# Kernel optimization log

Hardware: AMD Instinct MI355X
Metric: run time of the kernel (lower is better)

Reference implementation:

```python
import jax, jax.numpy as jnp
import numpy as np

N_NODES = 50000
N_EDGES = 1600000
NFEAT = 512
NHID = 64
H1 = 8      # nheads[0]
H2 = 1      # nheads[1]
NCLASS = 16
ALPHA = 0.2  # leaky_relu negative slope


def setup_inputs() -> dict:
    key = jax.random.key(0)
    ks = jax.random.split(key, 6)
    x = jax.random.normal(ks[0], (N_NODES, NFEAT), jnp.float32)
    edge_index = jax.random.randint(ks[1], (2, N_EDGES), 0, N_NODES, jnp.int32)

    def glorot(k, shape):
        fan_in, fan_out = shape[-2], shape[-1]
        std = (2.0 / (fan_in + fan_out)) ** 0.5
        return jax.random.normal(k, shape, jnp.float32) * std

    W1 = glorot(ks[2], (H1, NFEAT, NHID))
    a1 = jax.random.normal(ks[3], (H1, 2 * NHID), jnp.float32) * 0.1
    W2 = glorot(ks[4], (H2, NHID * H1, NCLASS))
    a2 = jax.random.normal(ks[5], (H2, 2 * NCLASS), jnp.float32) * 0.1
    return {"x": x, "edge_index": edge_index, "W1": W1, "a1": a1, "W2": W2, "a2": a2}


def _spgat_head(x, W, a, src, dst, n_nodes, apply_elu):
    # Sparse GAT head (pyGAT SpGraphAttentionLayer, eval mode / no dropout).
    h = x @ W                              # [N, F']
    f = W.shape[1]
    # a . [h_src || h_dst] decomposed into per-node scores (same math, no [E,2F'] concat)
    s_src = h @ a[:f]                      # [N]
    s_dst = h @ a[f:]                      # [N]
    logits = s_src[src] + s_dst[dst]       # [E]
    e = jnp.exp(-jax.nn.leaky_relu(logits, ALPHA))  # edge_e = exp(-leakyrelu(...)) > 0
    rowsum = jax.ops.segment_sum(e, src, num_segments=n_nodes)            # [N]
    agg = jax.ops.segment_sum(e[:, None] * h[dst], src, num_segments=n_nodes)  # [N, F']
    h_prime = agg / rowsum[:, None]
    return jax.nn.elu(h_prime) if apply_elu else h_prime


def reference(x, edge_index, W1, a1, W2, a2):
    src, dst = edge_index[0], edge_index[1]
    n = x.shape[0]
    # Layer 1: H1 heads, concat=True (elu inside each head), concatenated on features
    h = jnp.concatenate(
        [_spgat_head(x, W1[i], a1[i], src, dst, n, True) for i in range(W1.shape[0])],
        axis=1,
    )  # [N, H1*NHID]
    # Layer 2: H2 heads, concat=False, stacked then averaged
    outs = jnp.stack(
        [_spgat_head(h, W2[i], a2[i], src, dst, n, False) for i in range(W2.shape[0])],
        axis=2,
    )  # [N, NCLASS, H2]
    out = jnp.mean(outs, axis=2)
    return jax.nn.log_softmax(jax.nn.elu(out), axis=1)
```

## Files before the change

### kernel.cpp

```cpp
#include <hip/hip_runtime.h>

#define NN 50000
#define NE 1600000
#define NFEAT 512
#define NHID 64
#define H1 8
#define NCLASS 16
#define ALPHA 0.2f

#define BUCKETS 391
#define CAP 6144
#define EPB 4096
#define PASSA_BLKS 391
#define PASSB_BLKS 391
#define PACK_BLKS 1024
#define PACK2_BLKS 32
#define X8_BLKS 6250
#define GEMMB 391
#define NROW_PAD 50048

typedef __attribute__((ext_vector_type(8))) short short8;
typedef __attribute__((ext_vector_type(4))) float floatx4;
typedef __attribute__((ext_vector_type(2))) float floatx2;
typedef __attribute__((ext_vector_type(2))) long longx2;

__device__ __forceinline__ float elu_f(float x) { return x > 0.0f ? x : expf(x) - 1.0f; }
__device__ __forceinline__ float edge_w(float logit) {
    return expf(-fmaxf(logit, ALPHA * logit));
}
__device__ __forceinline__ ushort f2bf(float f) {
    uint u = __float_as_uint(f);
    return (ushort)((u + 0x7FFFu + ((u >> 16) & 1)) >> 16);
}
__device__ __forceinline__ uint packbf2(float lo, float hi) {
    return (uint)f2bf(lo) | ((uint)f2bf(hi) << 16);
}
__device__ __forceinline__ float bf2f(ushort v) { return __uint_as_float((uint)v << 16); }
__device__ __forceinline__ unsigned char f2fp8(float v) {
    return (unsigned char)(__builtin_amdgcn_cvt_pk_fp8_f32(v, v, 0, false) & 0xFF);
}
__device__ __forceinline__ uint pack4fp8(float a, float b, float c, float d) {
    uint u = __builtin_amdgcn_cvt_pk_fp8_f32(a, b, 0, false);
    return __builtin_amdgcn_cvt_pk_fp8_f32(c, d, u, true);
}

#define GLD16(g, l)                                                              \
    __builtin_amdgcn_global_load_lds(                                            \
        (const __attribute__((address_space(1))) unsigned int*)(g),              \
        (__attribute__((address_space(3))) unsigned int*)(l), 16, 0, 0)

__device__ __forceinline__ int scan256x(int v, int tid, int* wsum, int* tot) {
    int s = v;
#pragma unroll
    for (int o = 1; o < 64; o <<= 1) {
        int u = __shfl_up(s, o);
        if ((tid & 63) >= o) s += u;
    }
    __syncthreads();
    if ((tid & 63) == 63) wsum[tid >> 6] = s;
    __syncthreads();
    int off = 0, t = 0;
#pragma unroll
    for (int i = 0; i < 4; i++) {
        int x = wsum[i];
        if (i < (tid >> 6)) off += x;
        t += x;
    }
    *tot = t;
    return s - v + off;
}

__device__ __forceinline__ int scan512x(int v, int tid, int* wsum, int* tot) {
    int s = v;
#pragma unroll
    for (int o = 1; o < 64; o <<= 1) {
        int u = __shfl_up(s, o);
        if ((tid & 63) >= o) s += u;
    }
    __syncthreads();
    if ((tid & 63) == 63) wsum[tid >> 6] = s;
    __syncthreads();
    int off = 0, t = 0;
#pragma unroll
    for (int i = 0; i < 8; i++) {
        int x = wsum[i];
        if (i < (tid >> 6)) off += x;
        t += x;
    }
    *tot = t;
    return s - v + off;
}

__global__ __launch_bounds__(256) void prep_k(const float* __restrict__ W1,
                                              unsigned char* __restrict__ Wt8,
                                              const float* __restrict__ W2,
                                              ushort* __restrict__ W2tb,
                                              const float* __restrict__ x,
                                              unsigned char* x8,
                                              const int* __restrict__ ei,
                                              int* __restrict__ bucket_cnt,
                                              uint* __restrict__ staging) {
    int b = blockIdx.x;
    if (b < PACK_BLKS) {
        int i = b * 256 + threadIdx.x;
        int c = i >> 9, o = i & 511;
        int c6 = o >> 6, qhi = (o >> 4) & 3, kb = (o >> 3) & 1, bb = o & 7;
        int quad = qhi ^ ((c >> 1) & 3);
        int k = c6 * 64 + kb * 32 + quad * 8 + bb;
        Wt8[i] = f2fp8(W1[((c >> 6) * 512 + k) * 64 + (c & 63)]);
        return;
    }
    if (b < PACK_BLKS + PACK2_BLKS) {
        int i = (b - PACK_BLKS) * 256 + threadIdx.x;
        int c = i >> 9, f = i & 511;
        W2tb[i] = f2bf(W2[f * 16 + c]);
        return;
    }
    if (b < PACK_BLKS + PACK2_BLKS + X8_BLKS) {
        int i = (b - PACK_BLKS - PACK2_BLKS) * 256 + threadIdx.x;
        int row = i >> 5;
        int o0 = (i & 31) * 16;
        int c6 = o0 >> 6;
        int qhi = (o0 >> 4) & 3;
        int quad = qhi ^ ((row >> 1) & 3);
        const float* xp = x + (size_t)row * 512 + c6 * 64 + quad * 8;
        float4 v0 = *(const float4*)xp;
        float4 v1 = *(const float4*)(xp + 4);
        float4 v2 = *(const float4*)(xp + 32);
        float4 v3 = *(const float4*)(xp + 36);
        uint4 ov;
        ov.x = pack4fp8(v0.x, v0.y, v0.z, v0.w);
        ov.y = pack4fp8(v1.x, v1.y, v1.z, v1.w);
        ov.z = pack4fp8(v2.x, v2.y, v2.z, v2.w);
        ov.w = pack4fp8(v3.x, v3.y, v3.z, v3.w);
        *(uint4*)(x8 + (size_t)row * 512 + o0) = ov;
        return;
    }
    __shared__ int histA[BUCKETS];
    __shared__ int exclA[BUCKETS];
    __shared__ int baseA[BUCKETS];
    __shared__ int wsumA[4];
    __shared__ uint ebuf[EPB];
    const int blk = b - PACK_BLKS - PACK2_BLKS - X8_BLKS;
    const int t = threadIdx.x;
    const int e0 = blk * EPB;
    const int cntb = min(EPB, NE - e0);
    for (int i = t; i < BUCKETS; i += 256) histA[i] = 0;
    __syncthreads();
    int br[16]; uint pay[16];
#pragma unroll
    for (int i = 0; i < 16; i++) {
        int e = e0 + i * 256 + t;
        br[i] = -1;
        if (e < NE) {
            int s = ei[e], d = ei[NE + e];
            int bu = s >> 7;
            pay[i] = ((uint)bu << 23) | ((uint)(s & 127) << 16) | (uint)d;
            br[i] = (bu << 12) | atomicAdd(&histA[bu], 1);
        }
    }
    __syncthreads();
    int tot0, tot1;
    int v0 = histA[t];
    int v1 = (t + 256 < BUCKETS) ? histA[t + 256] : 0;
    int p0 = scan256x(v0, t, wsumA, &tot0);
    int p1 = scan256x(v1, t, wsumA, &tot1);
    exclA[t] = p0;
    if (t + 256 < BUCKETS) exclA[t + 256] = p1 + tot0;
    __syncthreads();
    for (int i = t; i < BUCKETS; i += 256) {
        int c = histA[i];
        if (c > 0) baseA[i] = atomicAdd(&bucket_cnt[i], c);
    }
#pragma unroll
    for (int i = 0; i < 16; i++)
        if (br[i] >= 0) ebuf[exclA[br[i] >> 12] + (br[i] & 4095)] = pay[i];
    __syncthreads();
    for (int j = t; j < cntb; j += 256) {
        uint v = ebuf[j];
        int bu = v >> 23;
        int pos = baseA[bu] + (j - exclA[bu]);
        staging[(size_t)bu * CAP + pos] = v;
    }
}

__global__ __launch_bounds__(64) void scan_k(const int* __restrict__ bucket_cnt,
                                             int* __restrict__ bucket_start,
                                             int* __restrict__ rowptr) {
    const int lane = threadIdx.x;
    int c[7]; int s0 = 0;
#pragma unroll
    for (int i = 0; i < 7; i++) {
        int b = lane * 7 + i;
        c[i] = (b < BUCKETS) ? bucket_cnt[b] : 0;
        s0 += c[i];
    }
    int sc = s0;
#pragma unroll
    for (int o = 1; o < 64; o <<= 1) {
        int u = __shfl_up(sc, o);
        if (lane >= o) sc += u;
    }
    int run = sc - s0;
#pragma unroll
    for (int i = 0; i < 7; i++) {
        int b = lane * 7 + i;
        if (b < BUCKETS) bucket_start[b] = run;
        run += c[i];
    }
    if (lane == 63) { bucket_start[BUCKETS] = run; rowptr[NN] = run; }
}

__global__ __launch_bounds__(512) void passb_gemm1_k(const int* __restrict__ bucket_cnt,
                                                     const int* __restrict__ bucket_start,
                                                     const uint* __restrict__ staging,
                                                     ushort* __restrict__ csru,
                                                     int* __restrict__ rowptr,
                                                     const unsigned char* __restrict__ Wt8,
                                                     const float* __restrict__ a1,
                                                     unsigned char* h8x8,
                                                     float* __restrict__ s1s,
                                                     float* __restrict__ s1d) {
    __shared__ unsigned char shmem[40960];
    const int tid = threadIdx.x;

    if (blockIdx.x < PASSB_BLKS) {
        int* hist2 = (int*)shmem;
        int* excl2 = hist2 + 128;
        int* cur2 = excl2 + 128;
        int* wsum2 = cur2 + 128;
        const int b = blockIdx.x;
        const int cnt = bucket_cnt[b];
        const int sbase = bucket_start[b];
        const uint* sg = staging + (size_t)b * CAP;
        if (tid < 128) { hist2[tid] = 0; cur2[tid] = 0; }
        __syncthreads();
        for (int e = tid; e < cnt; e += 512) atomicAdd(&hist2[(sg[e] >> 16) & 127], 1);
        __syncthreads();
        int v = (tid < 128) ? hist2[tid] : 0;
        int tot;
        int ex = scan512x(v, tid, wsum2, &tot);
        if (tid < 128) {
            excl2[tid] = ex;
            int n = b * 128 + tid;
            if (n < NN) rowptr[n] = sbase + ex;
        }
        __syncthreads();
        for (int e = tid; e < cnt; e += 512) {
            uint u = sg[e];
            int sl = (u >> 16) & 127;
            int pos = excl2[sl] + atomicAdd(&cur2[sl], 1);
            csru[sbase + pos] = (ushort)(u & 0xFFFF);
        }
        return;
    }

    unsigned char* As = shmem;
    unsigned char* Bs = shmem + 8192;
    const int gb = blockIdx.x - PASSB_BLKS;
    const int row0 = gb * 128;
    const int wv = tid >> 6, lane = tid & 63;
    const int l16 = lane & 15, quad = lane >> 4;
    const int qoff = ((quad ^ ((l16 >> 1) & 3)) << 4);
    const int mA = wv * 16 + (lane >> 2);
    const int offA = (lane & 3) * 16;
    const unsigned char* gA = h8x8 + (size_t)(row0 + mA) * 512 + offA;
    const unsigned char* gB0 = Wt8 + (size_t)(0 * 128 + mA) * 512 + offA;
    const unsigned char* gB1 = Wt8 + (size_t)(1 * 128 + mA) * 512 + offA;
    const unsigned char* gB2 = Wt8 + (size_t)(2 * 128 + mA) * 512 + offA;
    const unsigned char* gB3 = Wt8 + (size_t)(3 * 128 + mA) * 512 + offA;

    floatx4 acc[32];
#pragma unroll
    for (int ct = 0; ct < 32; ct++) acc[ct] = (floatx4){0.f, 0.f, 0.f, 0.f};

    for (int k0 = 0; k0 < 512; k0 += 64) {
        GLD16(gA + k0, As + wv * 1024);
        GLD16(gB0 + k0, Bs + wv * 1024);
        GLD16(gB1 + k0, Bs + 8192 + wv * 1024);
        GLD16(gB2 + k0, Bs + 16384 + wv * 1024);
        GLD16(gB3 + k0, Bs + 24576 + wv * 1024);
        __syncthreads();
        longx2 av = *(const longx2*)(As + (wv * 16 + l16) * 64 + qoff);
        const unsigned char* bp = Bs + l16 * 64 + qoff;
#pragma unroll
        for (int ct = 0; ct < 32; ct++) {
            longx2 bv = *(const longx2*)(bp + ct * 1024);
            acc[ct] = __builtin_amdgcn_mfma_f32_16x16x32_fp8_fp8(av.x, bv.x, acc[ct], 0, 0, 0);
            acc[ct] = __builtin_amdgcn_mfma_f32_16x16x32_fp8_fp8(av.y, bv.y, acc[ct], 0, 0, 0);
        }
        __syncthreads();
    }

    const int rbase = row0 + wv * 16 + quad * 4;
#pragma unroll
    for (int hh = 0; hh < 8; hh++) {
        float ss[4] = {0.f, 0.f, 0.f, 0.f}, sd[4] = {0.f, 0.f, 0.f, 0.f};
#pragma unroll
        for (int c4 = 0; c4 < 4; c4++) {
            int ct = hh * 4 + c4;
            int colg = ct * 16 + l16;
            float avs = a1[hh * 128 + c4 * 16 + l16];
            float avd = a1[hh * 128 + 64 + c4 * 16 + l16];
#pragma unroll
            for (int r = 0; r < 4; r++) {
                float v = acc[ct][r];
                ss[r] += v * avs;
                sd[r] += v * avd;
                int row = rbase + r;
                if (row < NN) h8x8[(size_t)row * 512 + colg] = f2fp8(v);
            }
        }
#pragma unroll
        for (int r = 0; r < 4; r++) {
            float a_ = ss[r], b_ = sd[r];
#pragma unroll
            for (int o = 1; o < 16; o <<= 1) {
                a_ += __shfl_xor(a_, o);
                b_ += __shfl_xor(b_, o);
            }
            int row = rbase + r;
            if (l16 == 0 && row < NN) {
                s1s[row * 8 + hh] = a_;
                s1d[row * 8 + hh] = b_;
            }
        }
    }
}

__global__ __launch_bounds__(256) void agg1f_k(const int* __restrict__ rowptr,
                                               const ushort* __restrict__ csru,
                                               const float* __restrict__ s1s,
                                               const float* __restrict__ s1d,
                                               const uint2* __restrict__ hb8,
                                               const ushort* __restrict__ W2tb,
                                               const float* __restrict__ a2,
                                               ushort* __restrict__ h2b,
                                               float* __restrict__ s2s,
                                               float* __restrict__ s2d) {
    __shared__ ushort Ash[16 * 512];
    const int tid = threadIdx.x;
    const int wv = tid >> 6, lane = tid & 63;
    const int n0 = blockIdx.x * 4;
    const int n = n0 + wv;
    const int head8 = lane >> 3;
    const int esub = lane & 7;
    const int beg = rowptr[n];
    const int deg = rowptr[n + 1] - beg;
    const float ssrc = s1s[n * 8 + head8];
    floatx2 acc[4] = {};
    float rsum = 0.f;

    int k = 0;
    for (; k + 8 <= deg; k += 8) {
        int dA = csru[beg + k + esub];
        float wA = edge_w(ssrc + s1d[dA * 8 + head8]);
        rsum += wA;
        int dj[8];
#pragma unroll
        for (int j = 0; j < 8; j++) dj[j] = __shfl(dA, j);
        uint2 v[8];
#pragma unroll
        for (int j = 0; j < 8; j++) v[j] = hb8[(uint)dj[j] * 64 + lane];
#pragma unroll
        for (int j = 0; j < 8; j++) {
            float wj = __shfl(wA, (head8 << 3) + j);
            floatx2 w2 = (floatx2){wj, wj};
            acc[0] += w2 * __builtin_amdgcn_cvt_pk_f32_fp8(v[j].x, false);
            acc[1] += w2 * __builtin_amdgcn_cvt_pk_f32_fp8(v[j].x, true);
            acc[2] += w2 * __builtin_amdgcn_cvt_pk_f32_fp8(v[j].y, false);
            acc[3] += w2 * __builtin_amdgcn_cvt_pk_f32_fp8(v[j].y, true);
        }
    }
    if (k < deg) {
        int jc = min(k + esub, deg - 1);
        int dwj = csru[beg + jc];
        float w = edge_w(ssrc + s1d[dwj * 8 + head8]);
        if (k + esub >= deg) w = 0.f;
        rsum += w;
        int rem = deg - k;
        for (int j = 0; j < rem; j++) {
            int djs = __shfl(dwj, j);
            uint2 vv = hb8[(uint)djs * 64 + lane];
            float wj = __shfl(w, (head8 << 3) + j);
            floatx2 w2 = (floatx2){wj, wj};
            acc[0] += w2 * __builtin_amdgcn_cvt_pk_f32_fp8(vv.x, false);
            acc[1] += w2 * __builtin_amdgcn_cvt_pk_f32_fp8(vv.x, true);
            acc[2] += w2 * __builtin_amdgcn_cvt_pk_f32_fp8(vv.y, false);
            acc[3] += w2 * __builtin_amdgcn_cvt_pk_f32_fp8(vv.y, true);
        }
    }

    rsum += __shfl_xor(rsum, 1);
    rsum += __shfl_xor(rsum, 2);
    rsum += __shfl_xor(rsum, 4);
    float inv = 1.0f / rsum;
    uint4 o;
    o.x = packbf2(elu_f(acc[0][0] * inv), elu_f(acc[0][1] * inv));
    o.y = packbf2(elu_f(acc[1][0] * inv), elu_f(acc[1][1] * inv));
    o.z = packbf2(elu_f(acc[2][0] * inv), elu_f(acc[2][1] * inv));
    o.w = packbf2(elu_f(acc[3][0] * inv), elu_f(acc[3][1] * inv));
    *(uint4*)(Ash + wv * 512 + lane * 8) = o;
    __syncthreads();

    if (wv == 0) {
        const int l16 = lane & 15, q = lane >> 4;
        floatx4 c2 = (floatx4){0.f, 0.f, 0.f, 0.f};
#pragma unroll
        for (int s = 0; s < 16; s++) {
            short8 af = *(const short8*)(Ash + l16 * 512 + s * 32 + q * 8);
            short8 bf = *(const short8*)(W2tb + l16 * 512 + s * 32 + q * 8);
            c2 = __builtin_amdgcn_mfma_f32_16x16x32_bf16(af, bf, c2, 0, 0, 0);
        }
        if (q == 0) {
#pragma unroll
            for (int r = 0; r < 4; r++) h2b[(size_t)(n0 + r) * 16 + l16] = f2bf(c2[r]);
        }
#pragma unroll
        for (int r = 0; r < 4; r++) {
            float ssv = c2[r] * a2[l16];
            float sdv = c2[r] * a2[16 + l16];
#pragma unroll
            for (int oo = 1; oo < 16; oo <<= 1) {
                ssv += __shfl_xor(ssv, oo);
                sdv += __shfl_xor(sdv, oo);
            }
            if (lane == 0) { s2s[n0 + r] = ssv; s2d[n0 + r] = sdv; }
        }
    }
}

__global__ __launch_bounds__(256) void agg2_k(const int* __restrict__ rowptr,
                                              const ushort* __restrict__ csru,
                                              const float* __restrict__ s2s,
                                              const float* __restrict__ s2d,
                                              const ushort* __restrict__ h2b,
                                              float* __restrict__ out) {
    const int n = (blockIdx.x * 256 + threadIdx.x) >> 6;
    const int lane = threadIdx.x & 63;
    if (n >= NN) return;
    const int beg = rowptr[n], end = rowptr[n + 1];
    const float sn = s2s[n];
    const int sub = lane >> 4, f = lane & 15;
    float acc = 0.f, rsum = 0.f;
    int e = beg + sub;
    for (; e + 12 < end; e += 16) {
        int d0 = csru[e], d1 = csru[e + 4], d2 = csru[e + 8], d3 = csru[e + 12];
        float t0 = s2d[d0], t1 = s2d[d1], t2 = s2d[d2], t3 = s2d[d3];
        float g0 = bf2f(h2b[(uint)d0 * 16 + f]), g1 = bf2f(h2b[(uint)d1 * 16 + f]);
        float g2 = bf2f(h2b[(uint)d2 * 16 + f]), g3 = bf2f(h2b[(uint)d3 * 16 + f]);
        float w0 = edge_w(sn + t0), w1 = edge_w(sn + t1);
        float w2 = edge_w(sn + t2), w3 = edge_w(sn + t3);
        acc += w0 * g0 + w1 * g1 + w2 * g2 + w3 * g3;
        rsum += w0 + w1 + w2 + w3;
    }
    for (; e < end; e += 4) {
        int d0 = csru[e];
        float w0 = edge_w(sn + s2d[d0]);
        acc += w0 * bf2f(h2b[(uint)d0 * 16 + f]);
        rsum += w0;
    }
    acc += __shfl_down(acc, 32);
    acc += __shfl_down(acc, 16);
    rsum += __shfl_down(rsum, 32);
    rsum += __shfl_down(rsum, 16);
    if (lane < 16) {
        float v = elu_f(acc / rsum);
        float m = v;
#pragma unroll
        for (int o = 8; o > 0; o >>= 1) m = fmaxf(m, __shfl_xor(m, o));
        float ex = expf(v - m), s = ex;
#pragma unroll
        for (int o = 8; o > 0; o >>= 1) s += __shfl_xor(s, o);
        out[(size_t)n * 16 + f] = v - (logf(s) + m);
    }
}

extern "C" void kernel_launch(void* const* d_in, const int* in_sizes, int n_in,
                              void* d_out, int out_size, void* d_ws, size_t ws_size,
                              hipStream_t stream) {
    const float* x  = (const float*)d_in[0];
    const int*   ei = (const int*)d_in[1];
    const float* W1 = (const float*)d_in[2];
    const float* a1 = (const float*)d_in[3];
    const float* W2 = (const float*)d_in[4];
    const float* a2 = (const float*)d_in[5];
    float* out = (float*)d_out;

    unsigned char* h8  = (unsigned char*)d_ws;
    unsigned char* Wt8 = h8 + (size_t)NROW_PAD * 512;
    ushort* W2tb  = (ushort*)(Wt8 + 512 * 512);
    float* s1s    = (float*)(W2tb + 8192);
    float* s1d    = s1s + (size_t)NN * H1;
    int* rowptr   = (int*)(s1d + (size_t)NN * H1);
    int* bucket_cnt   = rowptr + 50056;
    int* bucket_start = bucket_cnt + 512;
    ushort* csru  = (ushort*)(bucket_start + 512);
    ushort* h2b   = csru + NE;
    float* s2s    = (float*)(h2b + (size_t)NN * 16);
    float* s2d    = s2s + NN;
    uint* staging = (uint*)(s2d + NN);

    hipMemsetAsync(bucket_cnt, 0, 512 * sizeof(int), stream);

    prep_k<<<PACK_BLKS + PACK2_BLKS + X8_BLKS + PASSA_BLKS, 256, 0, stream>>>(
        W1, Wt8, W2, W2tb, x, h8, ei, bucket_cnt, staging);
    scan_k<<<1, 64, 0, stream>>>(bucket_cnt, bucket_start, rowptr);
    passb_gemm1_k<<<PASSB_BLKS + GEMMB, 512, 0, stream>>>(bucket_cnt, bucket_start,
                                                          staging, csru, rowptr,
                                                          Wt8, a1, h8, s1s, s1d);
    agg1f_k<<<NN / 4, 256, 0, stream>>>(rowptr, csru, s1s, s1d,
                                        (const uint2*)h8, W2tb, a2, h2b, s2s, s2d);
    agg2_k<<<(NN + 3) / 4, 256, 0, stream>>>(rowptr, csru, s2s, s2d, h2b, out);
}
```

Measured before the change: 401.4 us.

## Double-buffer edge gathers in layer-1 aggregation, swizzle LDS, use fast exp/log

The layer-1 aggregation loop is software-pipelined. It prefetches the next group of 8 neighbour indices, attention scores and fp8 feature rows into a second register buffer while the current group is accumulated, so gather latency overlaps with the FMA work. The LDS tile that feeds the second-layer MFMA now uses an XOR-swizzled layout to reduce bank conflicts on the strided row reads. expf and logf are also replaced by the __expf and __logf intrinsics. In exchange, the kernel uses more registers for the doubled gather buffers, which may lower occupancy, and the fast math intrinsics are slightly less accurate.

```diff
diff --git a/kernel.cpp b/kernel.cpp
--- a/kernel.cpp
+++ b/kernel.cpp
@@ -24,9 +24,9 @@
 typedef __attribute__((ext_vector_type(2))) float floatx2;
 typedef __attribute__((ext_vector_type(2))) long longx2;
 
-__device__ __forceinline__ float elu_f(float x) { return x > 0.0f ? x : expf(x) - 1.0f; }
+__device__ __forceinline__ float elu_f(float x) { return x > 0.0f ? x : __expf(x) - 1.0f; }
 __device__ __forceinline__ float edge_w(float logit) {
-    return expf(-fmaxf(logit, ALPHA * logit));
+    return __expf(-fmaxf(logit, ALPHA * logit));
 }
 __device__ __forceinline__ ushort f2bf(float f) {
     uint u = __float_as_uint(f);
@@ -328,6 +328,30 @@
     }
 }
 
+#define PREF8(gg, dN, twN, vN)                                        \
+    {                                                                 \
+        int idx_ = ((gg) < G) ? beg + (gg) * 8 + esub : beg;          \
+        dN = csru[idx_];                                              \
+        twN = s1d[dN * 8 + head8];                                    \
+        _Pragma("unroll") for (int j_ = 0; j_ < 8; j_++) {            \
+            int dj_ = __shfl(dN, j_);                                 \
+            vN[j_] = hb8[(uint)dj_ * 64 + lane];                      \
+        }                                                             \
+    }
+
+#define COMP8(wC, vC)                                                             \
+    {                                                                             \
+        rsum += wC;                                                               \
+        _Pragma("unroll") for (int j_ = 0; j_ < 8; j_++) {                        \
+            float wj_ = __shfl(wC, hb + j_);                                      \
+            floatx2 w2_ = (floatx2){wj_, wj_};                                    \
+            acc[0] += w2_ * __builtin_amdgcn_cvt_pk_f32_fp8(vC[j_].x, false);     \
+            acc[1] += w2_ * __builtin_amdgcn_cvt_pk_f32_fp8(vC[j_].x, true);      \
+            acc[2] += w2_ * __builtin_amdgcn_cvt_pk_f32_fp8(vC[j_].y, false);     \
+            acc[3] += w2_ * __builtin_amdgcn_cvt_pk_f32_fp8(vC[j_].y, true);      \
+        }                                                                         \
+    }
+
 __global__ __launch_bounds__(256) void agg1f_k(const int* __restrict__ rowptr,
                                                const ushort* __restrict__ csru,
                                                const float* __restrict__ s1s,
@@ -339,11 +363,13 @@
                                                float* __restrict__ s2s,
                                                float* __restrict__ s2d) {
     __shared__ ushort Ash[16 * 512];
+    unsigned char* ashb = (unsigned char*)Ash;
     const int tid = threadIdx.x;
     const int wv = tid >> 6, lane = tid & 63;
     const int n0 = blockIdx.x * 4;
     const int n = n0 + wv;
     const int head8 = lane >> 3;
+    const int hb = head8 << 3;
     const int esub = lane & 7;
     const int beg = rowptr[n];
     const int deg = rowptr[n + 1] - beg;
@@ -351,26 +377,24 @@
     floatx2 acc[4] = {};
     float rsum = 0.f;
 
-    int k = 0;
-    for (; k + 8 <= deg; k += 8) {
-        int dA = csru[beg + k + esub];
-        float wA = edge_w(ssrc + s1d[dA * 8 + head8]);
-        rsum += wA;
-        int dj[8];
-#pragma unroll
-        for (int j = 0; j < 8; j++) dj[j] = __shfl(dA, j);
-        uint2 v[8];
-#pragma unroll
-        for (int j = 0; j < 8; j++) v[j] = hb8[(uint)dj[j] * 64 + lane];
-#pragma unroll
-        for (int j = 0; j < 8; j++) {
-            float wj = __shfl(wA, (head8 << 3) + j);
-            floatx2 w2 = (floatx2){wj, wj};
-            acc[0] += w2 * __builtin_amdgcn_cvt_pk_f32_fp8(v[j].x, false);
-            acc[1] += w2 * __builtin_amdgcn_cvt_pk_f32_fp8(v[j].x, true);
-            acc[2] += w2 * __builtin_amdgcn_cvt_pk_f32_fp8(v[j].y, false);
-            acc[3] += w2 * __builtin_amdgcn_cvt_pk_f32_fp8(v[j].y, true);
-        }
+    const int G = deg >> 3;
+    int k = G << 3;
+    if (G > 0) {
+        int dA0, dA1;
+        float tw0, tw1, w0;
+        uint2 va[8], vb[8];
+        PREF8(0, dA0, tw0, va);
+        w0 = edge_w(ssrc + tw0);
+        int g = 0;
+        for (; g + 2 <= G; g += 2) {
+            PREF8(g + 1, dA1, tw1, vb);
+            COMP8(w0, va);
+            float w1 = edge_w(ssrc + tw1);
+            PREF8(g + 2, dA0, tw0, va);
+            COMP8(w1, vb);
+            w0 = edge_w(ssrc + tw0);
+        }
+        if (g < G) COMP8(w0, va);
     }
     if (k < deg) {
         int jc = min(k + esub, deg - 1);
@@ -382,7 +406,7 @@
         for (int j = 0; j < rem; j++) {
             int djs = __shfl(dwj, j);
             uint2 vv = hb8[(uint)djs * 64 + lane];
-            float wj = __shfl(w, (head8 << 3) + j);
+            float wj = __shfl(w, hb + j);
             floatx2 w2 = (floatx2){wj, wj};
             acc[0] += w2 * __builtin_amdgcn_cvt_pk_f32_fp8(vv.x, false);
             acc[1] += w2 * __builtin_amdgcn_cvt_pk_f32_fp8(vv.x, true);
@@ -400,7 +424,7 @@
     o.y = packbf2(elu_f(acc[1][0] * inv), elu_f(acc[1][1] * inv));
     o.z = packbf2(elu_f(acc[2][0] * inv), elu_f(acc[2][1] * inv));
     o.w = packbf2(elu_f(acc[3][0] * inv), elu_f(acc[3][1] * inv));
-    *(uint4*)(Ash + wv * 512 + lane * 8) = o;
+    *(uint4*)(ashb + wv * 1024 + ((lane * 16) ^ (wv << 4))) = o;
     __syncthreads();
 
     if (wv == 0) {
@@ -408,7 +432,8 @@
         floatx4 c2 = (floatx4){0.f, 0.f, 0.f, 0.f};
 #pragma unroll
         for (int s = 0; s < 16; s++) {
-            short8 af = *(const short8*)(Ash + l16 * 512 + s * 32 + q * 8);
+            short8 af = *(const short8*)(ashb + l16 * 1024 +
+                                         ((s * 64 + q * 16) ^ ((l16 & 7) << 4)));
             short8 bf = *(const short8*)(W2tb + l16 * 512 + s * 32 + q * 8);
             c2 = __builtin_amdgcn_mfma_f32_16x16x32_bf16(af, bf, c2, 0, 0, 0);
         }
@@ -469,10 +494,10 @@
         float m = v;
 #pragma unroll
         for (int o = 8; o > 0; o >>= 1) m = fmaxf(m, __shfl_xor(m, o));
-        float ex = expf(v - m), s = ex;
+        float ex = __expf(v - m), s = ex;
 #pragma unroll
         for (int o = 8; o > 0; o >>= 1) s += __shfl_xor(s, o);
-        out[(size_t)n * 16 + f] = v - (logf(s) + m);
+        out[(size_t)n * 16 + f] = v - (__logf(s) + m);
     }
 }
 
```

Result: slower. 411.6 us (+2.5%).
